# Optimization experiments

Hardware: AMD Instinct MI355X
Metric: run time of the kernel (lower is better)

Reference implementation:

```python
import jax, jax.numpy as jnp
import numpy as np

B = 65536
NUM_INPUTS = 256
NUM_HIDDEN = 256


def setup_inputs() -> dict:
    key = jax.random.key(0)
    ks = jax.random.split(key, 11)
    f32 = jnp.float32
    return {
        "x": jax.random.normal(ks[0], (B, NUM_INPUTS), dtype=f32),
        "h_t_1": jax.random.normal(ks[1], (B, NUM_HIDDEN), dtype=f32),
        "Wz": jax.random.normal(ks[2], (NUM_INPUTS, NUM_HIDDEN), dtype=f32),
        "Uz": jax.random.normal(ks[3], (NUM_HIDDEN, NUM_HIDDEN), dtype=f32),
        "bz": jax.random.normal(ks[4], (NUM_HIDDEN,), dtype=f32),
        "Wr": jax.random.normal(ks[5], (NUM_INPUTS, NUM_HIDDEN), dtype=f32),
        "Ur": jax.random.normal(ks[6], (NUM_HIDDEN, NUM_HIDDEN), dtype=f32),
        "br": jax.random.normal(ks[7], (NUM_HIDDEN,), dtype=f32),
        "Wh": jax.random.normal(ks[8], (NUM_INPUTS, NUM_HIDDEN), dtype=f32),
        "Uh": jax.random.normal(ks[9], (NUM_HIDDEN, NUM_HIDDEN), dtype=f32),
        "bh": jax.random.normal(ks[10], (NUM_HIDDEN,), dtype=f32),
    }


def reference(x, h_t_1, Wz, Uz, bz, Wr, Ur, br, Wh, Uh, bh):
    # update gate z = sigmoid(x@Wz + h@Uz + bz)
    z = jax.nn.sigmoid(x @ Wz + h_t_1 @ Uz + bz)
    # reset gate r = sigmoid(x@Wr + h@Ur + br)
    r = jax.nn.sigmoid(x @ Wr + h_t_1 @ Ur + br)
    # candidate: tanh(x@Wh + (r*h)@Uh + bh)
    h_hat = jnp.tanh(x @ Wh + (r * h_t_1) @ Uh + bh)
    h_t = z * h_t_1 + (1.0 - z) * h_hat
    return (h_t, h_t)
```

## Files before the change

kernel.cpp:

```cpp
#include <hip/hip_runtime.h>
#include <hip/hip_fp16.h>


#define NHID 256
#define B_ROWS 65536
#define MT 64
#define GATE_STRIDE (16 * 16 * 64 * 8)

typedef _Float16 half8 __attribute__((ext_vector_type(8)));
typedef _Float16 half4_t __attribute__((ext_vector_type(4)));
typedef float floatx4 __attribute__((ext_vector_type(4)));

__device__ __forceinline__ int lidx(int m, int c) {
    return m * 256 + ((((c >> 3) ^ (m & 7)) << 3)) + (c & 7);
}

__global__ __launch_bounds__(256) void pack_weights_kernel(
    const float* __restrict__ Wz, const float* __restrict__ Uz,
    const float* __restrict__ Wr, const float* __restrict__ Ur,
    const float* __restrict__ Wh, const float* __restrict__ Uh,
    _Float16* __restrict__ packed)
{
    int tid = blockIdx.x * blockDim.x + threadIdx.x;
    int lane = tid & 63;
    int s    = (tid >> 6) & 15;
    int ct   = (tid >> 10) & 15;
    int g    = tid >> 14;
    const float* W = (g == 0) ? Wz : (g == 1) ? Wr : Wh;
    const float* U = (g == 0) ? Uz : (g == 1) ? Ur : Uh;
    int n  = ct * 16 + (lane & 15);
    int k0 = s * 32 + (lane >> 4) * 8;
    half8 v;
#pragma unroll
    for (int j = 0; j < 8; ++j) {
        int k = k0 + j;
        float f = (k < 256) ? W[k * 256 + n] : U[(k - 256) * 256 + n];
        v[j] = (_Float16)f;
    }
    *reinterpret_cast<half8*>(packed + (size_t)tid * 8) = v;
}

__global__ __launch_bounds__(256, 2) void gru_main_kernel(
    const float* __restrict__ x, const float* __restrict__ h,
    const _Float16* __restrict__ wpack,
    const float* __restrict__ bz, const float* __restrict__ br,
    const float* __restrict__ bh,
    float* __restrict__ out)
{
    __shared__ _Float16 lx[MT * 256];
    __shared__ _Float16 lh[MT * 256];

    const int tid  = threadIdx.x;
    const int lane = tid & 63;
    const int wave = tid >> 6;
    const int row0 = blockIdx.x * MT;
    const int m_lo = lane & 15;
    const int quad = lane >> 4;

    {
        const float4* xv = reinterpret_cast<const float4*>(x + (size_t)row0 * NHID);
        const float4* hv = reinterpret_cast<const float4*>(h + (size_t)row0 * NHID);
#pragma unroll
        for (int it = 0; it < (MT * 64) / 256; ++it) {
            int i = it * 256 + tid;
            int m = i >> 6;
            int c = (i & 63) * 4;
            float4 a = xv[i];
            float4 b = hv[i];
            half4_t va = { (_Float16)a.x, (_Float16)a.y, (_Float16)a.z, (_Float16)a.w };
            half4_t vb = { (_Float16)b.x, (_Float16)b.y, (_Float16)b.z, (_Float16)b.w };
            *reinterpret_cast<half4_t*>(&lx[lidx(m, c)]) = va;
            *reinterpret_cast<half4_t*>(&lh[lidx(m, c)]) = vb;
        }
    }
    __syncthreads();

    const _Float16* wz = wpack;
    const _Float16* wr = wpack + GATE_STRIDE;
    const _Float16* wh = wpack + 2 * GATE_STRIDE;

    floatx4 accz[4][4];
    floatx4 accr[4][4];
#pragma unroll
    for (int c = 0; c < 4; ++c)
#pragma unroll
        for (int rt = 0; rt < 4; ++rt) {
            accz[c][rt] = (floatx4){0.f, 0.f, 0.f, 0.f};
            accr[c][rt] = (floatx4){0.f, 0.f, 0.f, 0.f};
        }

    const int mx = m_lo & 7;
#pragma unroll
    for (int s = 0; s < 16; ++s) {
        const _Float16* asrc = (s < 8) ? lx : lh;
        const int kcx = (((s & 7) * 4 + quad) ^ mx) << 3;
        half8 af[4];
#pragma unroll
        for (int rt = 0; rt < 4; ++rt)
            af[rt] = *reinterpret_cast<const half8*>(&asrc[(rt * 16 + m_lo) * 256 + kcx]);
#pragma unroll
        for (int c = 0; c < 4; ++c) {
            const int ct = wave * 4 + c;
            half8 bzf = *reinterpret_cast<const half8*>(&wz[(size_t)((ct * 16 + s) * 64 + lane) * 8]);
            half8 brf = *reinterpret_cast<const half8*>(&wr[(size_t)((ct * 16 + s) * 64 + lane) * 8]);
#pragma unroll
            for (int rt = 0; rt < 4; ++rt) {
                accz[c][rt] = __builtin_amdgcn_mfma_f32_16x16x32_f16(af[rt], bzf, accz[c][rt], 0, 0, 0);
                accr[c][rt] = __builtin_amdgcn_mfma_f32_16x16x32_f16(af[rt], brf, accr[c][rt], 0, 0, 0);
            }
        }
    }

    __syncthreads();

#pragma unroll
    for (int c = 0; c < 4; ++c) {
        const int col = wave * 64 + c * 16 + m_lo;
        const float bzv = bz[col];
        const float brv = br[col];
#pragma unroll
        for (int rt = 0; rt < 4; ++rt) {
#pragma unroll
            for (int e = 0; e < 4; ++e) {
                const int row = rt * 16 + quad * 4 + e;
                float sz = accz[c][rt][e] + bzv;
                float sr = accr[c][rt][e] + brv;
                float zv = 1.f / (1.f + __expf(-sz));
                float rv = 1.f / (1.f + __expf(-sr));
                const int li = lidx(row, col);
                float hval = (float)lh[li];
                lh[li] = (_Float16)(rv * hval);
                accz[c][rt][e] = zv * hval;
                accr[c][rt][e] = 1.f - zv;
            }
        }
    }
    __syncthreads();

    floatx4 acch[4][4];
#pragma unroll
    for (int c = 0; c < 4; ++c)
#pragma unroll
        for (int rt = 0; rt < 4; ++rt)
            acch[c][rt] = (floatx4){0.f, 0.f, 0.f, 0.f};

#pragma unroll
    for (int s = 0; s < 16; ++s) {
        const _Float16* asrc = (s < 8) ? lx : lh;
        const int kcx = (((s & 7) * 4 + quad) ^ mx) << 3;
        half8 af[4];
#pragma unroll
        for (int rt = 0; rt < 4; ++rt)
            af[rt] = *reinterpret_cast<const half8*>(&asrc[(rt * 16 + m_lo) * 256 + kcx]);
#pragma unroll
        for (int c = 0; c < 4; ++c) {
            const int ct = wave * 4 + c;
            half8 bhf = *reinterpret_cast<const half8*>(&wh[(size_t)((ct * 16 + s) * 64 + lane) * 8]);
#pragma unroll
            for (int rt = 0; rt < 4; ++rt)
                acch[c][rt] = __builtin_amdgcn_mfma_f32_16x16x32_f16(af[rt], bhf, acch[c][rt], 0, 0, 0);
        }
    }

    const size_t OUT2 = (size_t)B_ROWS * NHID;
#pragma unroll
    for (int c = 0; c < 4; ++c) {
        const int col = wave * 64 + c * 16 + m_lo;
        const float bhv = bh[col];
#pragma unroll
        for (int rt = 0; rt < 4; ++rt) {
#pragma unroll
            for (int e = 0; e < 4; ++e) {
                const int row = rt * 16 + quad * 4 + e;
                float sh = acch[c][rt][e] + bhv;
                float e2 = __expf(2.f * sh);
                float hh = 1.f - 2.f / (e2 + 1.f);
                float ht = accz[c][rt][e] + accr[c][rt][e] * hh;
                size_t idx = (size_t)(row0 + row) * NHID + col;
                out[idx] = ht;
                out[OUT2 + idx] = ht;
            }
        }
    }
}

extern "C" void kernel_launch(void* const* d_in, const int* in_sizes, int n_in,
                              void* d_out, int out_size, void* d_ws, size_t ws_size,
                              hipStream_t stream) {
    (void)in_sizes; (void)n_in; (void)out_size; (void)ws_size;
    const float* x  = (const float*)d_in[0];
    const float* h  = (const float*)d_in[1];
    const float* Wz = (const float*)d_in[2];
    const float* Uz = (const float*)d_in[3];
    const float* bz = (const float*)d_in[4];
    const float* Wr = (const float*)d_in[5];
    const float* Ur = (const float*)d_in[6];
    const float* br = (const float*)d_in[7];
    const float* Wh = (const float*)d_in[8];
    const float* Uh = (const float*)d_in[9];
    const float* bh = (const float*)d_in[10];
    float* out = (float*)d_out;
    _Float16* wpack = (_Float16*)d_ws;

    pack_weights_kernel<<<192, 256, 0, stream>>>(Wz, Uz, Wr, Ur, Wh, Uh, wpack);
    gru_main_kernel<<<B_ROWS / MT, 256, 0, stream>>>(x, h, wpack, bz, br, bh, out);
}
```

Before: 372.0 us.

## Halve row tile, raise occupancy, and stage outputs through LDS for vector stores

Cuts the rows per block from 64 to 32, which halves the accumulator register arrays, and raises the launch-bounds occupancy hint from 2 to 4 blocks per CU. The final h_t values are written into a padded LDS buffer that reuses the x/h staging space, then stored to global memory as coalesced float4 writes to both outputs instead of scattered scalar stores. In exchange, each block now reuses the weight fragments it loads across fewer rows, roughly doubling global/L2 weight traffic, and an extra LDS round trip with barriers is added.

```diff
diff --git a/kernel.cpp b/kernel.cpp
--- a/kernel.cpp
+++ b/kernel.cpp
@@ -4,7 +4,8 @@
 
 #define NHID 256
 #define B_ROWS 65536
-#define MT 64
+#define MT 32
+#define RT 2
 #define GATE_STRIDE (16 * 16 * 64 * 8)
 
 typedef _Float16 half8 __attribute__((ext_vector_type(8)));
@@ -40,15 +41,17 @@
     *reinterpret_cast<half8*>(packed + (size_t)tid * 8) = v;
 }
 
-__global__ __launch_bounds__(256, 2) void gru_main_kernel(
+__global__ __launch_bounds__(256, 4) void gru_main_kernel(
     const float* __restrict__ x, const float* __restrict__ h,
     const _Float16* __restrict__ wpack,
     const float* __restrict__ bz, const float* __restrict__ br,
     const float* __restrict__ bh,
     float* __restrict__ out)
 {
-    __shared__ _Float16 lx[MT * 256];
-    __shared__ _Float16 lh[MT * 256];
+    __shared__ __align__(16) unsigned char smem[MT * 260 * 4];
+    _Float16* lx = reinterpret_cast<_Float16*>(smem);
+    _Float16* lh = lx + MT * 256;
+    float* lout = reinterpret_cast<float*>(smem);
 
     const int tid  = threadIdx.x;
     const int lane = tid & 63;
@@ -79,12 +82,12 @@
     const _Float16* wr = wpack + GATE_STRIDE;
     const _Float16* wh = wpack + 2 * GATE_STRIDE;
 
-    floatx4 accz[4][4];
-    floatx4 accr[4][4];
+    floatx4 accz[4][RT];
+    floatx4 accr[4][RT];
 #pragma unroll
     for (int c = 0; c < 4; ++c)
 #pragma unroll
-        for (int rt = 0; rt < 4; ++rt) {
+        for (int rt = 0; rt < RT; ++rt) {
             accz[c][rt] = (floatx4){0.f, 0.f, 0.f, 0.f};
             accr[c][rt] = (floatx4){0.f, 0.f, 0.f, 0.f};
         }
@@ -94,9 +97,9 @@
     for (int s = 0; s < 16; ++s) {
         const _Float16* asrc = (s < 8) ? lx : lh;
         const int kcx = (((s & 7) * 4 + quad) ^ mx) << 3;
-        half8 af[4];
-#pragma unroll
-        for (int rt = 0; rt < 4; ++rt)
+        half8 af[RT];
+#pragma unroll
+        for (int rt = 0; rt < RT; ++rt)
             af[rt] = *reinterpret_cast<const half8*>(&asrc[(rt * 16 + m_lo) * 256 + kcx]);
 #pragma unroll
         for (int c = 0; c < 4; ++c) {
@@ -104,7 +107,7 @@
             half8 bzf = *reinterpret_cast<const half8*>(&wz[(size_t)((ct * 16 + s) * 64 + lane) * 8]);
             half8 brf = *reinterpret_cast<const half8*>(&wr[(size_t)((ct * 16 + s) * 64 + lane) * 8]);
 #pragma unroll
-            for (int rt = 0; rt < 4; ++rt) {
+            for (int rt = 0; rt < RT; ++rt) {
                 accz[c][rt] = __builtin_amdgcn_mfma_f32_16x16x32_f16(af[rt], bzf, accz[c][rt], 0, 0, 0);
                 accr[c][rt] = __builtin_amdgcn_mfma_f32_16x16x32_f16(af[rt], brf, accr[c][rt], 0, 0, 0);
             }
@@ -119,7 +122,7 @@
         const float bzv = bz[col];
         const float brv = br[col];
 #pragma unroll
-        for (int rt = 0; rt < 4; ++rt) {
+        for (int rt = 0; rt < RT; ++rt) {
 #pragma unroll
             for (int e = 0; e < 4; ++e) {
                 const int row = rt * 16 + quad * 4 + e;
@@ -137,50 +140,60 @@
     }
     __syncthreads();
 
-    floatx4 acch[4][4];
+    floatx4 acch[4][RT];
 #pragma unroll
     for (int c = 0; c < 4; ++c)
 #pragma unroll
-        for (int rt = 0; rt < 4; ++rt)
+        for (int rt = 0; rt < RT; ++rt)
             acch[c][rt] = (floatx4){0.f, 0.f, 0.f, 0.f};
 
 #pragma unroll
     for (int s = 0; s < 16; ++s) {
         const _Float16* asrc = (s < 8) ? lx : lh;
         const int kcx = (((s & 7) * 4 + quad) ^ mx) << 3;
-        half8 af[4];
-#pragma unroll
-        for (int rt = 0; rt < 4; ++rt)
+        half8 af[RT];
+#pragma unroll
+        for (int rt = 0; rt < RT; ++rt)
             af[rt] = *reinterpret_cast<const half8*>(&asrc[(rt * 16 + m_lo) * 256 + kcx]);
 #pragma unroll
         for (int c = 0; c < 4; ++c) {
             const int ct = wave * 4 + c;
             half8 bhf = *reinterpret_cast<const half8*>(&wh[(size_t)((ct * 16 + s) * 64 + lane) * 8]);
 #pragma unroll
-            for (int rt = 0; rt < 4; ++rt)
+            for (int rt = 0; rt < RT; ++rt)
                 acch[c][rt] = __builtin_amdgcn_mfma_f32_16x16x32_f16(af[rt], bhf, acch[c][rt], 0, 0, 0);
         }
     }
-
-    const size_t OUT2 = (size_t)B_ROWS * NHID;
+    __syncthreads();
+
 #pragma unroll
     for (int c = 0; c < 4; ++c) {
         const int col = wave * 64 + c * 16 + m_lo;
         const float bhv = bh[col];
 #pragma unroll
-        for (int rt = 0; rt < 4; ++rt) {
+        for (int rt = 0; rt < RT; ++rt) {
 #pragma unroll
             for (int e = 0; e < 4; ++e) {
                 const int row = rt * 16 + quad * 4 + e;
                 float sh = acch[c][rt][e] + bhv;
                 float e2 = __expf(2.f * sh);
                 float hh = 1.f - 2.f / (e2 + 1.f);
-                float ht = accz[c][rt][e] + accr[c][rt][e] * hh;
-                size_t idx = (size_t)(row0 + row) * NHID + col;
-                out[idx] = ht;
-                out[OUT2 + idx] = ht;
+                lout[row * 260 + col] = accz[c][rt][e] + accr[c][rt][e] * hh;
             }
         }
+    }
+    __syncthreads();
+
+    const size_t OUT2 = (size_t)B_ROWS * NHID;
+#pragma unroll
+    for (int it = 0; it < (MT * 64) / 256; ++it) {
+        int i = it * 256 + tid;
+        int m = i >> 6;
+        int cv = (i & 63) * 4;
+        float4 v = *reinterpret_cast<const float4*>(&lout[m * 260 + cv]);
+        size_t idx = (size_t)(row0 + m) * NHID + cv;
+        *reinterpret_cast<float4*>(&out[idx]) = v;
+        *reinterpret_cast<float4*>(&out[OUT2 + idx]) = v;
     }
 }
 
```

Result: slower. 380.9 us (+2.4%).
